# Kernel tuning notes

Hardware: AMD Instinct MI355X
Metric: run time of the kernel (lower is better)

## Reference

```python
import jax, jax.numpy as jnp
import numpy as np

HR, WR = 2, 2  # height_reduction, width_reduction


def setup_inputs() -> dict:
    key = jax.random.key(0)
    k1, k2, k3 = jax.random.split(key, 3)
    b, c, h, w = 16, 64, 512, 512
    images = jax.random.normal(k1, (b, c, h, w), dtype=jnp.float32)
    # per (batch, channel) sub-pixel offsets in [0, reduction)
    p_w = jax.random.randint(k2, (b, c), 0, WR, dtype=jnp.int32)
    p_h = jax.random.randint(k3, (b, c), 0, HR, dtype=jnp.int32)
    return {"images": images, "p_w": p_w, "p_h": p_h}


def reference(images, p_w, p_h):
    b, c, h, w = images.shape
    out_h, out_w = h // HR, w // WR
    # block start coordinates per output pixel, clamped like block_pool
    y_starts = jnp.clip(p_h[:, :, None] + jnp.arange(0, h, HR), 0, h - HR)  # [b,c,out_h]
    x_starts = jnp.clip(p_w[:, :, None] + jnp.arange(0, w, WR), 0, w - WR)  # [b,c,out_w]
    # expand to all pixels inside each block and flatten
    y_idx = (y_starts[..., None] + jnp.arange(HR)).reshape(b, c, out_h * HR)  # [b,c,out_h*HR]
    x_idx = (x_starts[..., None] + jnp.arange(WR)).reshape(b, c, out_w * WR)  # [b,c,out_w*WR]
    # gather rows then columns (two 1-D gathers instead of a 2-D gather)
    rows = jnp.take_along_axis(images, y_idx[:, :, :, None], axis=2)          # [b,c,out_h*HR,w]
    blocks = jnp.take_along_axis(rows, x_idx[:, :, None, :], axis=3)         # [b,c,out_h*HR,out_w*WR]
    blocks = blocks.reshape(b, c, out_h, HR, out_w, WR)
    return blocks.max(axis=(3, 5))  # [b,c,out_h,out_w]
```

## Files before the change

### kernel.cpp

```cpp
#include <hip/hip_runtime.h>


#define H 512
#define W 512
#define OH 256
#define OW 256

__global__ __launch_bounds__(256) void equivariant_subsample_kernel(
    const float* __restrict__ img,
    const int* __restrict__ p_w,
    const int* __restrict__ p_h,
    float* __restrict__ out)
{
    const int t  = threadIdx.x;
    const int bc = blockIdx.x >> 6;
    const int oy = ((blockIdx.x & 63) << 2) + threadIdx.y;

    const int ph = p_h[bc];
    const int pw = p_w[bc];

    int y0 = ph + 2 * oy;
    if (y0 > H - 2) y0 = H - 2;

    const float* row0 = img + ((size_t)bc * H + (size_t)y0) * W;
    const float* row1 = row0 + W;

    const float4 a0 = *(const float4*)(row0 + 8 * t);
    const float4 b0 = *(const float4*)(row0 + 8 * t + 4);
    const float4 a1 = *(const float4*)(row1 + 8 * t);
    const float4 b1 = *(const float4*)(row1 + 8 * t + 4);

    float4 r;
    if (pw == 0) {
        r.x = fmaxf(fmaxf(a0.x, a0.y), fmaxf(a1.x, a1.y));
        r.y = fmaxf(fmaxf(a0.z, a0.w), fmaxf(a1.z, a1.w));
        r.z = fmaxf(fmaxf(b0.x, b0.y), fmaxf(b1.x, b1.y));
        r.w = fmaxf(fmaxf(b0.z, b0.w), fmaxf(b1.z, b1.w));
    } else {
        const float e0 = __shfl_down(a0.x, 1);
        const float e1 = __shfl_down(a1.x, 1);
        r.x = fmaxf(fmaxf(a0.y, a0.z), fmaxf(a1.y, a1.z));
        r.y = fmaxf(fmaxf(a0.w, b0.x), fmaxf(a1.w, b1.x));
        r.z = fmaxf(fmaxf(b0.y, b0.z), fmaxf(b1.y, b1.z));
        if (t == 63) {
            r.w = fmaxf(fmaxf(b0.z, b0.w), fmaxf(b1.z, b1.w));
        } else {
            r.w = fmaxf(fmaxf(b0.w, e0), fmaxf(b1.w, e1));
        }
    }

    float4* o = (float4*)(out + ((size_t)bc * OH + (size_t)oy) * OW + 4 * t);
    *o = r;
}

extern "C" void kernel_launch(void* const* d_in, const int* in_sizes, int n_in,
                              void* d_out, int out_size, void* d_ws, size_t ws_size,
                              hipStream_t stream) {
    const float* img = (const float*)d_in[0];
    const int* pw = (const int*)d_in[1];
    const int* ph = (const int*)d_in[2];
    float* out = (float*)d_out;

    dim3 grid(16 * 64 * 64);
    dim3 block(64, 4);
    equivariant_subsample_kernel<<<grid, block, 0, stream>>>(img, pw, ph, out);
}
```

Baseline: 1.405 ms.

## Process four output rows per wave with split-half coalesced float4 loads

```diff
diff --git a/kernel.cpp b/kernel.cpp
--- a/kernel.cpp
+++ b/kernel.cpp
@@ -13,44 +13,70 @@
     float* __restrict__ out)
 {
     const int t  = threadIdx.x;
-    const int bc = blockIdx.x >> 6;
-    const int oy = ((blockIdx.x & 63) << 2) + threadIdx.y;
+    const int wy = threadIdx.y;
+    const int bc = blockIdx.x >> 4;
+    const int oy0 = ((blockIdx.x & 15) << 4) + (wy << 2);
 
     const int ph = p_h[bc];
     const int pw = p_w[bc];
 
-    int y0 = ph + 2 * oy;
-    if (y0 > H - 2) y0 = H - 2;
+    const float* __restrict__ base = img + (size_t)bc * (H * W);
+    float* __restrict__ obase = out + (size_t)bc * (OH * OW);
 
-    const float* row0 = img + ((size_t)bc * H + (size_t)y0) * W;
-    const float* row1 = row0 + W;
+    float4 v0[4], v1[4], v2[4], v3[4];
+    #pragma unroll
+    for (int r = 0; r < 4; ++r) {
+        int y0 = ph + 2 * (oy0 + r);
+        if (y0 > H - 2) y0 = H - 2;
+        const float* row0 = base + (size_t)y0 * W;
+        v0[r] = *(const float4*)(row0 + 4 * t);
+        v1[r] = *(const float4*)(row0 + 256 + 4 * t);
+        v2[r] = *(const float4*)(row0 + W + 4 * t);
+        v3[r] = *(const float4*)(row0 + W + 256 + 4 * t);
+    }
 
-    const float4 a0 = *(const float4*)(row0 + 8 * t);
-    const float4 b0 = *(const float4*)(row0 + 8 * t + 4);
-    const float4 a1 = *(const float4*)(row1 + 8 * t);
-    const float4 b1 = *(const float4*)(row1 + 8 * t + 4);
+    if (pw == 0) {
+        #pragma unroll
+        for (int r = 0; r < 4; ++r) {
+            float2 h0, h1;
+            h0.x = fmaxf(fmaxf(v0[r].x, v0[r].y), fmaxf(v2[r].x, v2[r].y));
+            h0.y = fmaxf(fmaxf(v0[r].z, v0[r].w), fmaxf(v2[r].z, v2[r].w));
+            h1.x = fmaxf(fmaxf(v1[r].x, v1[r].y), fmaxf(v3[r].x, v3[r].y));
+            h1.y = fmaxf(fmaxf(v1[r].z, v1[r].w), fmaxf(v3[r].z, v3[r].w));
+            float* orow = obase + (size_t)(oy0 + r) * OW;
+            *(float2*)(orow + 2 * t)       = h0;
+            *(float2*)(orow + 128 + 2 * t) = h1;
+        }
+    } else {
+        #pragma unroll
+        for (int r = 0; r < 4; ++r) {
+            const float n0 = __shfl_down(v0[r].x, 1);
+            const float n2 = __shfl_down(v2[r].x, 1);
+            const float n1 = __shfl_down(v1[r].x, 1);
+            const float n3 = __shfl_down(v3[r].x, 1);
+            const float m0 = __shfl(v1[r].x, 0);
+            const float m2 = __shfl(v3[r].x, 0);
 
-    float4 r;
-    if (pw == 0) {
-        r.x = fmaxf(fmaxf(a0.x, a0.y), fmaxf(a1.x, a1.y));
-        r.y = fmaxf(fmaxf(a0.z, a0.w), fmaxf(a1.z, a1.w));
-        r.z = fmaxf(fmaxf(b0.x, b0.y), fmaxf(b1.x, b1.y));
-        r.w = fmaxf(fmaxf(b0.z, b0.w), fmaxf(b1.z, b1.w));
-    } else {
-        const float e0 = __shfl_down(a0.x, 1);
-        const float e1 = __shfl_down(a1.x, 1);
-        r.x = fmaxf(fmaxf(a0.y, a0.z), fmaxf(a1.y, a1.z));
-        r.y = fmaxf(fmaxf(a0.w, b0.x), fmaxf(a1.w, b1.x));
-        r.z = fmaxf(fmaxf(b0.y, b0.z), fmaxf(b1.y, b1.z));
-        if (t == 63) {
-            r.w = fmaxf(fmaxf(b0.z, b0.w), fmaxf(b1.z, b1.w));
-        } else {
-            r.w = fmaxf(fmaxf(b0.w, e0), fmaxf(b1.w, e1));
+            float2 h0, h1;
+            h0.x = fmaxf(fmaxf(v0[r].y, v0[r].z), fmaxf(v2[r].y, v2[r].z));
+            {
+                const float e0 = (t == 63) ? m0 : n0;
+                const float e2 = (t == 63) ? m2 : n2;
+                h0.y = fmaxf(fmaxf(v0[r].w, e0), fmaxf(v2[r].w, e2));
+            }
+            h1.x = fmaxf(fmaxf(v1[r].y, v1[r].z), fmaxf(v3[r].y, v3[r].z));
+            {
+                const float a = (t == 63) ? v1[r].z : v1[r].w;
+                const float b = (t == 63) ? v1[r].w : n1;
+                const float c = (t == 63) ? v3[r].z : v3[r].w;
+                const float d = (t == 63) ? v3[r].w : n3;
+                h1.y = fmaxf(fmaxf(a, b), fmaxf(c, d));
+            }
+            float* orow = obase + (size_t)(oy0 + r) * OW;
+            *(float2*)(orow + 2 * t)       = h0;
+            *(float2*)(orow + 128 + 2 * t) = h1;
         }
     }
-
-    float4* o = (float4*)(out + ((size_t)bc * OH + (size_t)oy) * OW + 4 * t);
-    *o = r;
 }
 
 extern "C" void kernel_launch(void* const* d_in, const int* in_sizes, int n_in,
@@ -61,7 +87,7 @@
     const int* ph = (const int*)d_in[2];
     float* out = (float*)d_out;
 
-    dim3 grid(16 * 64 * 64);
+    dim3 grid(16 * 64 * 16);
     dim3 block(64, 4);
     equivariant_subsample_kernel<<<grid, block, 0, stream>>>(img, pw, ph, out);
 }
```

Result: no change. 1.410 ms (+0.4%).
